# Optimization experiments

Hardware: AMD Instinct MI355X
Metric: run time of the kernel (lower is better)

The kernel has to match this reference:

```python
import jax, jax.numpy as jnp
import numpy as np

TEMPERATURE = 0.07
TOP_MARGIN = 0.95
BOTTOM_MARGIN = 0.05

BATCH = 8192
DIM = 1024


def setup_inputs() -> dict:
    key = jax.random.key(0)
    kA, kB = jax.random.split(key)
    embedding_A = jax.random.normal(kA, (BATCH, DIM), dtype=jnp.float32)
    embedding_B = jax.random.normal(kB, (BATCH, DIM), dtype=jnp.float32)
    return {"embedding_A": embedding_A, "embedding_B": embedding_B}


def _l2norm(x):
    return x * jax.lax.rsqrt(jnp.sum(x * x, axis=-1, keepdims=True))


def reference(embedding_A, embedding_B):
    a = _l2norm(embedding_A)
    b = _l2norm(embedding_B)
    B = a.shape[0]
    sim = a @ b.T                                   # [B, B]
    pos = jnp.diagonal(sim)                         # [B]
    eye = jnp.eye(B, dtype=bool)
    upper = pos[:, None] * TOP_MARGIN
    lower = pos[:, None] * BOTTOM_MARGIN
    neg_mask = (sim <= upper) & (sim >= lower) & ~eye   # [B, B]

    # Per-row CE over [positive, hard negatives] == masked logsumexp - pos/tau.
    z = sim / TEMPERATURE
    full_mask = neg_mask | eye                      # positive always included
    masked = jnp.where(full_mask, z, -jnp.inf)
    m = jnp.max(masked, axis=1, keepdims=True)      # finite: diag always present
    lse = m[:, 0] + jnp.log(jnp.sum(jnp.exp(masked - m), axis=1))
    per_row = lse - pos / TEMPERATURE               # [B]

    valid = jnp.any(neg_mask, axis=1)               # rows with >=1 negative
    count = jnp.sum(valid)
    total = jnp.sum(jnp.where(valid, per_row, 0.0))
    return total / jnp.maximum(count, 1).astype(total.dtype)
```

## Files before the change

### kernel.cpp

```cpp
#include <hip/hip_runtime.h>
#include <hip/hip_bf16.h>

#define BATCH 8192
#define DIM   1024
#define INV_TAU (1.0f / 0.07f)
#define TOPM 0.95f
#define BOTM 0.05f

#define BM 256
#define BN 256
#define BK 64
#define NT (DIM / BK)

typedef __attribute__((ext_vector_type(4))) float f32x4;
typedef __attribute__((ext_vector_type(8))) short bf16x8;

typedef __attribute__((address_space(3))) void       lds_void_t;
typedef const __attribute__((address_space(1))) void gbl_void_t;

__device__ inline void async_copy16(const void* g, void* l) {
    __builtin_amdgcn_global_load_lds((gbl_void_t*)g, (lds_void_t*)l, 16, 0, 0);
}

__device__ inline unsigned short f2bf(float f) {
    __hip_bfloat16 h = __float2bfloat16(f);
    return *reinterpret_cast<unsigned short*>(&h);
}

__global__ __launch_bounds__(256) void prep_kernel(
    const float* __restrict__ A, const float* __restrict__ B,
    unsigned short* __restrict__ An, unsigned short* __restrict__ Bn,
    float* __restrict__ pos, float* __restrict__ S)
{
    int row = blockIdx.x;
    int t = threadIdx.x;
    const float4* a4 = (const float4*)(A + (size_t)row * DIM);
    const float4* b4 = (const float4*)(B + (size_t)row * DIM);
    float4 av = a4[t];
    float4 bv = b4[t];
    float sa = av.x*av.x + av.y*av.y + av.z*av.z + av.w*av.w;
    float sb = bv.x*bv.x + bv.y*bv.y + bv.z*bv.z + bv.w*bv.w;
    float dp = av.x*bv.x + av.y*bv.y + av.z*bv.z + av.w*bv.w;
    #pragma unroll
    for (int d = 32; d > 0; d >>= 1) {
        sa += __shfl_down(sa, d);
        sb += __shfl_down(sb, d);
        dp += __shfl_down(dp, d);
    }
    __shared__ float red[3][4];
    int lane = t & 63, w = t >> 6;
    if (lane == 0) { red[0][w] = sa; red[1][w] = sb; red[2][w] = dp; }
    __syncthreads();
    sa = red[0][0] + red[0][1] + red[0][2] + red[0][3];
    sb = red[1][0] + red[1][1] + red[1][2] + red[1][3];
    dp = red[2][0] + red[2][1] + red[2][2] + red[2][3];
    float ra = rsqrtf(sa);
    float rb = rsqrtf(sb);
    if (t == 0) {
        pos[row] = dp * ra * rb;
        S[row] = 0.0f;
    }
    ushort4 oa, ob;
    oa.x = f2bf(av.x * ra); oa.y = f2bf(av.y * ra);
    oa.z = f2bf(av.z * ra); oa.w = f2bf(av.w * ra);
    ob.x = f2bf(bv.x * rb); ob.y = f2bf(bv.y * rb);
    ob.z = f2bf(bv.z * rb); ob.w = f2bf(bv.w * rb);
    ((ushort4*)(An + (size_t)row * DIM))[t] = oa;
    ((ushort4*)(Bn + (size_t)row * DIM))[t] = ob;
}

__global__ __launch_bounds__(512, 2) void sim_loss_kernel(
    const unsigned short* __restrict__ An, const unsigned short* __restrict__ Bn,
    const float* __restrict__ pos, float* __restrict__ S)
{
    __shared__ char lds[131072];

    int tid  = threadIdx.x;
    int lane = tid & 63;
    int wave = tid >> 6;
    int wm = wave >> 2, wn = wave & 3;
    int fr = lane & 15;
    int q  = lane >> 4;

    int bid = blockIdx.x;
    int xcd = bid & 7, idx = bid >> 3, gen = idx >> 5, j = idx & 31;
    int qr = gen >> 1, qc = (gen & 1) ^ (qr & 1);
    int by = qr * 16 + (xcd >> 1) * 4 + (j >> 3);
    int bx = qc * 16 + (xcd & 1) * 8 + (j & 7);
    int rowBase = by * BM, colBase = bx * BN;

    f32x4 acc[8][4] = {};
    bf16x8 a[4][2];
    bf16x8 b[2][2][2];

    int sw = (fr & 7) << 4;
    int c0 = (q * 16) ^ sw;
    int c1 = (64 + q * 16) ^ sw;
    int aRow = (wm * 128 + fr) * 128;
    int bRow = (wn * 64 + fr) * 128;

    int strow = tid >> 3;
    int scb   = ((tid & 7) * 16) ^ ((strow & 7) << 4);
    const char* gA = (const char*)An + (size_t)(rowBase + strow) * 2048 + scb;
    const char* gB = (const char*)Bn + (size_t)(colBase + strow) * 2048 + scb;
    int ldst = tid * 16;

#define STAGE(gbase, u, h, ldsdst) do {                                              \
    async_copy16((gbase) + (size_t)(h) * 262144 + (size_t)(u) * 128,                 \
                 (ldsdst) + (h) * 16384 + ldst);                                     \
    async_copy16((gbase) + (size_t)(h) * 262144 + 131072 + (size_t)(u) * 128,        \
                 (ldsdst) + (h) * 16384 + 8192 + ldst);                              \
} while (0)

#define LDA(sAp, mh) do {                                                            \
    _Pragma("unroll") for (int m = 0; m < 4; ++m) {                                  \
        a[m][0] = *(const bf16x8*)((sAp) + aRow + (mh) * 8192 + m * 2048 + c0);      \
        a[m][1] = *(const bf16x8*)((sAp) + aRow + (mh) * 8192 + m * 2048 + c1);      \
    }                                                                                \
} while (0)

#define LDB(sBp, nh) do {                                                            \
    _Pragma("unroll") for (int n = 0; n < 2; ++n) {                                  \
        b[nh][n][0] = *(const bf16x8*)((sBp) + bRow + (nh) * 4096 + n * 2048 + c0);  \
        b[nh][n][1] = *(const bf16x8*)((sBp) + bRow + (nh) * 4096 + n * 2048 + c1);  \
    }                                                                                \
} while (0)

#define MM(mh, nh) do {                                                              \
    _Pragma("unroll") for (int m = 0; m < 4; ++m)                                    \
    _Pragma("unroll") for (int n = 0; n < 2; ++n) {                                  \
        acc[(mh)*4+m][(nh)*2+n] = __builtin_amdgcn_mfma_f32_16x16x32_bf16(           \
            a[m][0], b[nh][n][0], acc[(mh)*4+m][(nh)*2+n], 0, 0, 0);                 \
        acc[(mh)*4+m][(nh)*2+n] = __builtin_amdgcn_mfma_f32_16x16x32_bf16(           \
            a[m][1], b[nh][n][1], acc[(mh)*4+m][(nh)*2+n], 0, 0, 0);                 \
    }                                                                                \
} while (0)

#define BAR() __builtin_amdgcn_s_barrier()
#define SCH() __builtin_amdgcn_sched_barrier(0)
#define LGKM(n) do { asm volatile("s_waitcnt lgkmcnt(" #n ")" ::: "memory");         \
                     SCH(); } while (0)
#define VMC(n)  asm volatile("s_waitcnt vmcnt(" #n ")" ::: "memory")
#define PRI1() __builtin_amdgcn_s_setprio(1)
#define PRI0() __builtin_amdgcn_s_setprio(0)

#define KTILE(p, uA, uB) do {                                                        \
    const char* sAp = lds + (p) * 32768;                                             \
    const char* sBp = lds + 65536 + (p) * 32768;                                     \
    char* stA = lds + ((p) ^ 1) * 32768;                                             \
    char* stB = lds + 65536 + (p) * 32768;                                           \
                             \
    LDA(sAp, 0); LDB(sBp, 0); LDB(sBp, 1); STAGE(gA, (uA), 0, stA);                  \
    LGKM(4); PRI1(); MM(0, 0); PRI0(); BAR();                                        \
                                                                    \
    STAGE(gA, (uA), 1, stA);                                                         \
    LGKM(0); PRI1(); MM(0, 1); PRI0(); BAR(); SCH();                                 \
                                                               \
    LDA(sAp, 1); STAGE(gB, (uB), 0, stB);                                            \
    LGKM(0); PRI1(); MM(1, 1); PRI0(); BAR();                                        \
                                       \
    STAGE(gB, (uB), 1, stB);                                                         \
    PRI1(); MM(1, 0); PRI0(); VMC(4); BAR(); SCH();                                  \
} while (0)

    STAGE(gA, 0, 0, lds);
    STAGE(gA, 0, 1, lds);
    STAGE(gB, 0, 0, lds + 65536);
    STAGE(gB, 0, 1, lds + 65536);
    STAGE(gB, 1, 0, lds + 65536 + 32768);
    STAGE(gB, 1, 1, lds + 65536 + 32768);
    VMC(4);
    BAR();
    SCH();

    for (int tt = 0; tt < NT / 2; ++tt) {
        int t0 = tt * 2;
        { int uA = (t0 + 1) & 15, uB = (t0 + 2) & 15; KTILE(0, uA, uB); }
        { int uA = (t0 + 2) & 15, uB = (t0 + 3) & 15; KTILE(1, uA, uB); }
    }

    #pragma unroll
    for (int m = 0; m < 8; ++m) {
        #pragma unroll
        for (int j2 = 0; j2 < 4; ++j2) {
            int i = rowBase + wm * 128 + m * 16 + q * 4 + j2;
            float p  = pos[i];
            float up = TOPM * p, lo = BOTM * p;
            float rs = 0.0f;
            #pragma unroll
            for (int n = 0; n < 4; ++n) {
                float sv = acc[m][n][j2];
                int col = colBase + wn * 64 + n * 16 + fr;
                if (sv <= up && sv >= lo && col != i)
                    rs += __expf((sv - p) * INV_TAU);
            }
            #pragma unroll
            for (int d = 1; d < 16; d <<= 1)
                rs += __shfl_xor(rs, d);
            if (fr == 0 && rs != 0.0f)
                atomicAdd(&S[i], rs);
        }
    }
    VMC(0);
#undef STAGE
#undef LDA
#undef LDB
#undef MM
#undef BAR
#undef SCH
#undef LGKM
#undef VMC
#undef PRI1
#undef PRI0
#undef KTILE
}

__global__ __launch_bounds__(256) void finalize_kernel(
    const float* __restrict__ S, float* __restrict__ out)
{
    int t = threadIdx.x;
    float tot = 0.0f;
    int c = 0;
    for (int i = t; i < BATCH; i += 256) {
        float s = S[i];
        if (s > 0.0f) { tot += log1pf(s); c += 1; }
    }
    #pragma unroll
    for (int d = 32; d > 0; d >>= 1) {
        tot += __shfl_down(tot, d);
        c   += __shfl_down(c, d);
    }
    __shared__ float st[4];
    __shared__ int   sc[4];
    int lane = t & 63, w = t >> 6;
    if (lane == 0) { st[w] = tot; sc[w] = c; }
    __syncthreads();
    if (t == 0) {
        float T = st[0] + st[1] + st[2] + st[3];
        int   C = sc[0] + sc[1] + sc[2] + sc[3];
        out[0] = T / (float)(C > 0 ? C : 1);
    }
}

extern "C" void kernel_launch(void* const* d_in, const int* in_sizes, int n_in,
                              void* d_out, int out_size, void* d_ws, size_t ws_size,
                              hipStream_t stream) {
    const float* A = (const float*)d_in[0];
    const float* B = (const float*)d_in[1];

    char* ws = (char*)d_ws;
    unsigned short* An = (unsigned short*)ws;
    unsigned short* Bn = An + (size_t)BATCH * DIM;
    float* pos = (float*)(Bn + (size_t)BATCH * DIM);
    float* S   = pos + BATCH;
    float* out = (float*)d_out;

    prep_kernel<<<BATCH, 256, 0, stream>>>(A, B, An, Bn, pos, S);
    sim_loss_kernel<<<dim3(BATCH / BM * BATCH / BN), 512, 0, stream>>>(An, Bn, pos, S);
    finalize_kernel<<<1, 256, 0, stream>>>(S, out);
}
```

Baseline: 212.5 us.

## Make similarity kernel persistent, processing four tiles per block with cross-tile prefetch

Launches 256 persistent blocks that each compute four 256x256 similarity tiles sequentially, reusing the swizzled tile mapping. The next tile's first K panels are prefetched during the last K iterations of the current tile, hiding the pipeline prologue. Accumulators are reset after each tile's masked-exp epilogue. This trades away block-level parallelism, one block per CU instead of two, so epilogue and latency may be less hidden.

```diff
diff --git a/kernel.cpp b/kernel.cpp
--- a/kernel.cpp
+++ b/kernel.cpp
@@ -83,11 +83,13 @@
     int q  = lane >> 4;
 
     int bid = blockIdx.x;
-    int xcd = bid & 7, idx = bid >> 3, gen = idx >> 5, j = idx & 31;
-    int qr = gen >> 1, qc = (gen & 1) ^ (qr & 1);
-    int by = qr * 16 + (xcd >> 1) * 4 + (j >> 3);
-    int bx = qc * 16 + (xcd & 1) * 8 + (j & 7);
-    int rowBase = by * BM, colBase = bx * BN;
+
+#define BASES(g, rB, cB) do {                                                        \
+    int xcd_ = bid & 7, jj_ = bid >> 3;                                              \
+    int qr_ = (g) >> 1, qc_ = ((g) & 1) ^ (qr_ & 1);                                 \
+    (rB) = (qr_ * 16 + (xcd_ >> 1) * 4 + (jj_ >> 3)) * BM;                           \
+    (cB) = (qc_ * 16 + (xcd_ & 1) * 8 + (jj_ & 7)) * BN;                             \
+} while (0)
 
     f32x4 acc[8][4] = {};
     bf16x8 a[4][2];
@@ -101,9 +103,12 @@
 
     int strow = tid >> 3;
     int scb   = ((tid & 7) * 16) ^ ((strow & 7) << 4);
-    const char* gA = (const char*)An + (size_t)(rowBase + strow) * 2048 + scb;
-    const char* gB = (const char*)Bn + (size_t)(colBase + strow) * 2048 + scb;
     int ldst = tid * 16;
+
+#define PANELS(rB, cB, pA, pB) do {                                                  \
+    (pA) = (const char*)An + (size_t)((rB) + strow) * 2048 + scb;                    \
+    (pB) = (const char*)Bn + (size_t)((cB) + strow) * 2048 + scb;                    \
+} while (0)
 
 #define STAGE(gbase, u, h, ldsdst) do {                                              \
     async_copy16((gbase) + (size_t)(h) * 262144 + (size_t)(u) * 128,                 \
@@ -144,64 +149,90 @@
 #define PRI1() __builtin_amdgcn_s_setprio(1)
 #define PRI0() __builtin_amdgcn_s_setprio(0)
 
-#define KTILE(p, uA, uB) do {                                                        \
+#define KTILE(p, gA_, uA, gB_, uB) do {                                              \
     const char* sAp = lds + (p) * 32768;                                             \
     const char* sBp = lds + 65536 + (p) * 32768;                                     \
     char* stA = lds + ((p) ^ 1) * 32768;                                             \
     char* stB = lds + 65536 + (p) * 32768;                                           \
                              \
-    LDA(sAp, 0); LDB(sBp, 0); LDB(sBp, 1); STAGE(gA, (uA), 0, stA);                  \
+    LDA(sAp, 0); LDB(sBp, 0); LDB(sBp, 1); STAGE((gA_), (uA), 0, stA);               \
     LGKM(4); PRI1(); MM(0, 0); PRI0(); BAR();                                        \
                                                                     \
-    STAGE(gA, (uA), 1, stA);                                                         \
+    STAGE((gA_), (uA), 1, stA);                                                      \
     LGKM(0); PRI1(); MM(0, 1); PRI0(); BAR(); SCH();                                 \
                                                                \
-    LDA(sAp, 1); STAGE(gB, (uB), 0, stB);                                            \
+    LDA(sAp, 1); STAGE((gB_), (uB), 0, stB);                                         \
     LGKM(0); PRI1(); MM(1, 1); PRI0(); BAR();                                        \
-                                       \
-    STAGE(gB, (uB), 1, stB);                                                         \
+                                     \
+    STAGE((gB_), (uB), 1, stB);                                                      \
     PRI1(); MM(1, 0); PRI0(); VMC(4); BAR(); SCH();                                  \
 } while (0)
 
-    STAGE(gA, 0, 0, lds);
-    STAGE(gA, 0, 1, lds);
-    STAGE(gB, 0, 0, lds + 65536);
-    STAGE(gB, 0, 1, lds + 65536);
-    STAGE(gB, 1, 0, lds + 65536 + 32768);
-    STAGE(gB, 1, 1, lds + 65536 + 32768);
+    int rowB, colB;
+    BASES(0, rowB, colB);
+    const char *gAc, *gBc;
+    PANELS(rowB, colB, gAc, gBc);
+
+    STAGE(gAc, 0, 0, lds);
+    STAGE(gAc, 0, 1, lds);
+    STAGE(gBc, 0, 0, lds + 65536);
+    STAGE(gBc, 0, 1, lds + 65536);
+    STAGE(gBc, 1, 0, lds + 65536 + 32768);
+    STAGE(gBc, 1, 1, lds + 65536 + 32768);
     VMC(4);
     BAR();
     SCH();
 
-    for (int tt = 0; tt < NT / 2; ++tt) {
-        int t0 = tt * 2;
-        { int uA = (t0 + 1) & 15, uB = (t0 + 2) & 15; KTILE(0, uA, uB); }
-        { int uA = (t0 + 2) & 15, uB = (t0 + 3) & 15; KTILE(1, uA, uB); }
-    }
-
-    #pragma unroll
-    for (int m = 0; m < 8; ++m) {
+    #pragma unroll 1
+    for (int g = 0; g < 4; ++g) {
+        int gn = (g < 3) ? g + 1 : 3;
+        int rowBn, colBn;
+        BASES(gn, rowBn, colBn);
+        const char *gAn2, *gBn2;
+        PANELS(rowBn, colBn, gAn2, gBn2);
+
+        #pragma unroll 1
+        for (int tt = 0; tt < 7; ++tt) {
+            KTILE(0, gAc, 2 * tt + 1, gBc, 2 * tt + 2);
+            KTILE(1, gAc, 2 * tt + 2, gBc, 2 * tt + 3);
+        }
+        KTILE(0, gAc, 15, gBn2, 0);
+        KTILE(1, gAn2, 0, gBn2, 1);
+
         #pragma unroll
-        for (int j2 = 0; j2 < 4; ++j2) {
-            int i = rowBase + wm * 128 + m * 16 + q * 4 + j2;
-            float p  = pos[i];
-            float up = TOPM * p, lo = BOTM * p;
-            float rs = 0.0f;
+        for (int m = 0; m < 8; ++m) {
             #pragma unroll
-            for (int n = 0; n < 4; ++n) {
-                float sv = acc[m][n][j2];
-                int col = colBase + wn * 64 + n * 16 + fr;
-                if (sv <= up && sv >= lo && col != i)
-                    rs += __expf((sv - p) * INV_TAU);
+            for (int j2 = 0; j2 < 4; ++j2) {
+                int i = rowB + wm * 128 + m * 16 + q * 4 + j2;
+                float p  = pos[i];
+                float up = TOPM * p, lo = BOTM * p;
+                float rs = 0.0f;
+                #pragma unroll
+                for (int n = 0; n < 4; ++n) {
+                    float sv = acc[m][n][j2];
+                    int col = colB + wn * 64 + n * 16 + fr;
+                    if (sv <= up && sv >= lo && col != i)
+                        rs += __expf((sv - p) * INV_TAU);
+                }
+                #pragma unroll
+                for (int d = 1; d < 16; d <<= 1)
+                    rs += __shfl_xor(rs, d);
+                if (fr == 0 && rs != 0.0f)
+                    atomicAdd(&S[i], rs);
             }
+        }
+        #pragma unroll
+        for (int m2 = 0; m2 < 8; ++m2)
             #pragma unroll
-            for (int d = 1; d < 16; d <<= 1)
-                rs += __shfl_xor(rs, d);
-            if (fr == 0 && rs != 0.0f)
-                atomicAdd(&S[i], rs);
-        }
+            for (int n2 = 0; n2 < 4; ++n2)
+                acc[m2][n2] = (f32x4){0.0f, 0.0f, 0.0f, 0.0f};
+
+        gAc = gAn2; gBc = gBn2; rowB = rowBn; colB = colBn;
     }
     VMC(0);
+
+#undef BASES
+#undef PANELS
 #undef STAGE
 #undef LDA
 #undef LDB
@@ -256,6 +287,6 @@
     float* out = (float*)d_out;
 
     prep_kernel<<<BATCH, 256, 0, stream>>>(A, B, An, Bn, pos, S);
-    sim_loss_kernel<<<dim3(BATCH / BM * BATCH / BN), 512, 0, stream>>>(An, Bn, pos, S);
+    sim_loss_kernel<<<256, 512, 0, stream>>>(An, Bn, pos, S);
     finalize_kernel<<<1, 256, 0, stream>>>(S, out);
 }
```

Result: faster. 202.6 us (-4.7%).

## Shrink GEMM tile to 128x128 with simpler two-phase pipeline and XCD-aware mapping

Applied to the files above, without the earlier changes.

Halves the block tile from 256x256 to 128x128, with 4 waves along N and 2 along M. It also halves the LDS footprint and raises the occupancy hint to 4 blocks per CU. The per-K-tile schedule becomes a simpler two-phase loop, and the block-to-tile mapping is changed to a new XCD-grouped layout. The aim is better latency hiding through more resident blocks and shorter per-wave critical paths. The cost is double the global and LDS traffic per FLOP, plus a lower MFMA-to-load ratio per wave.

```diff
diff --git a/kernel.cpp b/kernel.cpp
--- a/kernel.cpp
+++ b/kernel.cpp
@@ -7,8 +7,8 @@
 #define TOPM 0.95f
 #define BOTM 0.05f
 
-#define BM 256
-#define BN 256
+#define BM 128
+#define BN 128
 #define BK 64
 #define NT (DIM / BK)
 
@@ -69,11 +69,11 @@
     ((ushort4*)(Bn + (size_t)row * DIM))[t] = ob;
 }
 
-__global__ __launch_bounds__(512, 2) void sim_loss_kernel(
+__global__ __launch_bounds__(512, 4) void sim_loss_kernel(
     const unsigned short* __restrict__ An, const unsigned short* __restrict__ Bn,
     const float* __restrict__ pos, float* __restrict__ S)
 {
-    __shared__ char lds[131072];
+    __shared__ char lds[65536];
 
     int tid  = threadIdx.x;
     int lane = tid & 63;
@@ -83,114 +83,105 @@
     int q  = lane >> 4;
 
     int bid = blockIdx.x;
-    int xcd = bid & 7, idx = bid >> 3, gen = idx >> 5, j = idx & 31;
-    int qr = gen >> 1, qc = (gen & 1) ^ (qr & 1);
-    int by = qr * 16 + (xcd >> 1) * 4 + (j >> 3);
-    int bx = qc * 16 + (xcd & 1) * 8 + (j & 7);
-    int rowBase = by * BM, colBase = bx * BN;
-
-    f32x4 acc[8][4] = {};
+    int xcd = bid & 7;
+    int s   = bid >> 3;
+    int g   = s >> 6;
+    int t5  = s & 63;
+    int by  = g * 8 + (t5 >> 3);
+    int bx  = xcd * 8 + (t5 & 7);
+    int rowB = by * BM, colB = bx * BN;
+
+    f32x4 acc[4][2] = {};
     bf16x8 a[4][2];
-    bf16x8 b[2][2][2];
+    bf16x8 b0[2];
+    bf16x8 b1[2];
 
     int sw = (fr & 7) << 4;
     int c0 = (q * 16) ^ sw;
     int c1 = (64 + q * 16) ^ sw;
-    int aRow = (wm * 128 + fr) * 128;
-    int bRow = (wn * 64 + fr) * 128;
+    int aRow = (wm * 64 + fr) * 128;
+    int bRow = (wn * 32 + fr) * 128;
 
     int strow = tid >> 3;
     int scb   = ((tid & 7) * 16) ^ ((strow & 7) << 4);
-    const char* gA = (const char*)An + (size_t)(rowBase + strow) * 2048 + scb;
-    const char* gB = (const char*)Bn + (size_t)(colBase + strow) * 2048 + scb;
     int ldst = tid * 16;
 
-#define STAGE(gbase, u, h, ldsdst) do {                                              \
-    async_copy16((gbase) + (size_t)(h) * 262144 + (size_t)(u) * 128,                 \
-                 (ldsdst) + (h) * 16384 + ldst);                                     \
-    async_copy16((gbase) + (size_t)(h) * 262144 + 131072 + (size_t)(u) * 128,        \
-                 (ldsdst) + (h) * 16384 + 8192 + ldst);                              \
-} while (0)
-
-#define LDA(sAp, mh) do {                                                            \
+    const char* gA = (const char*)An + (size_t)(rowB + strow) * 2048 + scb;
+    const char* gB = (const char*)Bn + (size_t)(colB + strow) * 2048 + scb;
+
+#define STAGE(gbase, u, ldsdst) do {                                                 \
+    async_copy16((gbase) + (size_t)(u) * 128, (ldsdst) + ldst);                      \
+    async_copy16((gbase) + 131072 + (size_t)(u) * 128, (ldsdst) + 8192 + ldst);      \
+} while (0)
+
+#define LDA_(p) do {                                                                 \
+    const char* _s = lds + (p) * 16384;                                              \
     _Pragma("unroll") for (int m = 0; m < 4; ++m) {                                  \
-        a[m][0] = *(const bf16x8*)((sAp) + aRow + (mh) * 8192 + m * 2048 + c0);      \
-        a[m][1] = *(const bf16x8*)((sAp) + aRow + (mh) * 8192 + m * 2048 + c1);      \
+        a[m][0] = *(const bf16x8*)(_s + aRow + m * 2048 + c0);                       \
+        a[m][1] = *(const bf16x8*)(_s + aRow + m * 2048 + c1);                       \
     }                                                                                \
 } while (0)
 
-#define LDB(sBp, nh) do {                                                            \
-    _Pragma("unroll") for (int n = 0; n < 2; ++n) {                                  \
-        b[nh][n][0] = *(const bf16x8*)((sBp) + bRow + (nh) * 4096 + n * 2048 + c0);  \
-        b[nh][n][1] = *(const bf16x8*)((sBp) + bRow + (nh) * 4096 + n * 2048 + c1);  \
-    }                                                                                \
-} while (0)
-
-#define MM(mh, nh) do {                                                              \
-    _Pragma("unroll") for (int m = 0; m < 4; ++m)                                    \
-    _Pragma("unroll") for (int n = 0; n < 2; ++n) {                                  \
-        acc[(mh)*4+m][(nh)*2+n] = __builtin_amdgcn_mfma_f32_16x16x32_bf16(           \
-            a[m][0], b[nh][n][0], acc[(mh)*4+m][(nh)*2+n], 0, 0, 0);                 \
-        acc[(mh)*4+m][(nh)*2+n] = __builtin_amdgcn_mfma_f32_16x16x32_bf16(           \
-            a[m][1], b[nh][n][1], acc[(mh)*4+m][(nh)*2+n], 0, 0, 0);                 \
+#define LDB_(arr, p, nh) do {                                                        \
+    const char* _s = lds + 32768 + (p) * 16384;                                      \
+    arr[0] = *(const bf16x8*)(_s + bRow + (nh) * 2048 + c0);                         \
+    arr[1] = *(const bf16x8*)(_s + bRow + (nh) * 2048 + c1);                         \
+} while (0)
+
+#define MM_(barr, no) do {                                                           \
+    _Pragma("unroll") for (int m = 0; m < 4; ++m) {                                  \
+        acc[m][no] = __builtin_amdgcn_mfma_f32_16x16x32_bf16(                        \
+            a[m][0], barr[0], acc[m][no], 0, 0, 0);                                  \
+        acc[m][no] = __builtin_amdgcn_mfma_f32_16x16x32_bf16(                        \
+            a[m][1], barr[1], acc[m][no], 0, 0, 0);                                  \
     }                                                                                \
 } while (0)
 
 #define BAR() __builtin_amdgcn_s_barrier()
 #define SCH() __builtin_amdgcn_sched_barrier(0)
-#define LGKM(n) do { asm volatile("s_waitcnt lgkmcnt(" #n ")" ::: "memory");         \
-                     SCH(); } while (0)
+#define LGKM0() asm volatile("s_waitcnt lgkmcnt(0)" ::: "memory")
 #define VMC(n)  asm volatile("s_waitcnt vmcnt(" #n ")" ::: "memory")
 #define PRI1() __builtin_amdgcn_s_setprio(1)
 #define PRI0() __builtin_amdgcn_s_setprio(0)
 
 #define KTILE(p, uA, uB) do {                                                        \
-    const char* sAp = lds + (p) * 32768;                                             \
-    const char* sBp = lds + 65536 + (p) * 32768;                                     \
-    char* stA = lds + ((p) ^ 1) * 32768;                                             \
-    char* stB = lds + 65536 + (p) * 32768;                                           \
-                             \
-    LDA(sAp, 0); LDB(sBp, 0); LDB(sBp, 1); STAGE(gA, (uA), 0, stA);                  \
-    LGKM(4); PRI1(); MM(0, 0); PRI0(); BAR();                                        \
-                                                                    \
-    STAGE(gA, (uA), 1, stA);                                                         \
-    LGKM(0); PRI1(); MM(0, 1); PRI0(); BAR(); SCH();                                 \
-                                                               \
-    LDA(sAp, 1); STAGE(gB, (uB), 0, stB);                                            \
-    LGKM(0); PRI1(); MM(1, 1); PRI0(); BAR();                                        \
-                                       \
-    STAGE(gB, (uB), 1, stB);                                                         \
-    PRI1(); MM(1, 0); PRI0(); VMC(4); BAR(); SCH();                                  \
-} while (0)
-
-    STAGE(gA, 0, 0, lds);
-    STAGE(gA, 0, 1, lds);
-    STAGE(gB, 0, 0, lds + 65536);
-    STAGE(gB, 0, 1, lds + 65536);
-    STAGE(gB, 1, 0, lds + 65536 + 32768);
-    STAGE(gB, 1, 1, lds + 65536 + 32768);
-    VMC(4);
-    BAR();
-    SCH();
-
-    for (int tt = 0; tt < NT / 2; ++tt) {
-        int t0 = tt * 2;
-        { int uA = (t0 + 1) & 15, uB = (t0 + 2) & 15; KTILE(0, uA, uB); }
-        { int uA = (t0 + 2) & 15, uB = (t0 + 3) & 15; KTILE(1, uA, uB); }
+    char* stA = lds + ((p) ^ 1) * 16384;                                             \
+    char* stB = lds + 32768 + (p) * 16384;                                           \
+    BAR(); SCH();                                                                    \
+    LDA_((p)); LDB_(b0, (p), 0); LDB_(b1, (p), 1);                                   \
+    STAGE(gA, (uA), stA);                                                            \
+    PRI1(); MM_(b0, 0); PRI0();                                                      \
+    LGKM0();                                                                         \
+    BAR(); SCH();                                                                    \
+    STAGE(gB, (uB), stB);                                                            \
+    PRI1(); MM_(b1, 1); PRI0();                                                      \
+    VMC(2);                                                                          \
+} while (0)
+
+    STAGE(gA, 0, lds);
+    STAGE(gB, 0, lds + 32768);
+    STAGE(gB, 1, lds + 49152);
+    VMC(2);
+
+    #pragma unroll 1
+    for (int tt = 0; tt < 8; ++tt) {
+        int t0 = 2 * tt;
+        KTILE(0, (t0 + 1) & 15, (t0 + 2) & 15);
+        KTILE(1, (t0 + 2) & 15, (t0 + 3) & 15);
     }
 
     #pragma unroll
-    for (int m = 0; m < 8; ++m) {
+    for (int m = 0; m < 4; ++m) {
         #pragma unroll
         for (int j2 = 0; j2 < 4; ++j2) {
-            int i = rowBase + wm * 128 + m * 16 + q * 4 + j2;
+            int i = rowB + wm * 64 + m * 16 + q * 4 + j2;
             float p  = pos[i];
             float up = TOPM * p, lo = BOTM * p;
             float rs = 0.0f;
             #pragma unroll
-            for (int n = 0; n < 4; ++n) {
+            for (int n = 0; n < 2; ++n) {
                 float sv = acc[m][n][j2];
-                int col = colBase + wn * 64 + n * 16 + fr;
+                int col = colB + wn * 32 + n * 16 + fr;
                 if (sv <= up && sv >= lo && col != i)
                     rs += __expf((sv - p) * INV_TAU);
             }
@@ -201,14 +192,16 @@
                 atomicAdd(&S[i], rs);
         }
     }
+    LGKM0();
     VMC(0);
+
 #undef STAGE
-#undef LDA
-#undef LDB
-#undef MM
+#undef LDA_
+#undef LDB_
+#undef MM_
 #undef BAR
 #undef SCH
-#undef LGKM
+#undef LGKM0
 #undef VMC
 #undef PRI1
 #undef PRI0
@@ -256,6 +249,6 @@
     float* out = (float*)d_out;
 
     prep_kernel<<<BATCH, 256, 0, stream>>>(A, B, An, Bn, pos, S);
-    sim_loss_kernel<<<dim3(BATCH / BM * BATCH / BN), 512, 0, stream>>>(An, Bn, pos, S);
+    sim_loss_kernel<<<(BATCH / BM) * (BATCH / BN), 512, 0, stream>>>(An, Bn, pos, S);
     finalize_kernel<<<1, 256, 0, stream>>>(S, out);
 }
```

New measurement: 276.4 us. 1.3x slower.
